# Kernel tuning notes

Hardware: AMD Instinct MI355X
Metric: run time of the kernel (lower is better)

The kernel has to match this reference:

```python
import jax, jax.numpy as jnp
import numpy as np

N_NODES = 100000
N_EDGES = 1600000
F_IN = 16
F_OUT = 16
N_BASIS = 4  # per spatial dim; basisTerms = [4, 4]


def linear_basis(u, n):
    """Piecewise-linear (hat) basis, n terms on [-1, 1]. u: [E] -> [E, n]."""
    centers = jnp.linspace(-1.0, 1.0, n, dtype=u.dtype)
    dx = 2.0 / (n - 1)
    return jnp.maximum(0.0, 1.0 - jnp.abs(u[:, None] - centers[None, :]) / dx)


def setup_inputs() -> dict:
    key = jax.random.key(0)
    k1, k2, k3, k4, k5 = jax.random.split(key, 5)
    x = jax.random.normal(k1, (N_NODES, F_IN), dtype=jnp.float32)
    edge_index = jax.random.randint(k2, (2, N_EDGES), 0, N_NODES, dtype=jnp.int64)
    # relative positions normalized to [-1, 1]^2 (as in initializeWeights2D)
    edge_attr = jax.random.uniform(k3, (N_EDGES, 2), dtype=jnp.float32,
                                   minval=-1.0, maxval=1.0)
    # weight: [*basisTerms, inputFeatures, outputFeatures], uniform(-0.05, 0.05)
    weight = jax.random.uniform(k4, (N_BASIS, N_BASIS, F_IN, F_OUT),
                                dtype=jnp.float32, minval=-0.05, maxval=0.05)
    return {"x": x, "edge_index": edge_index, "edge_attr": edge_attr,
            "weight": weight}


def reference(x, edge_index, edge_attr, weight):
    """BasisConvLayer forward, mode='conv', linear basis, no bias/activations.

    For each edge e=(i<-j): msg_e = sum_{u,v} b_u(dx) b_v(dy) * (x_j @ W[u,v]);
    out[i] = sum over incoming edges of msg_e.
    """
    row, col = edge_index[0], edge_index[1]
    x_j = x[col]                                   # [E, F_in] gather
    bx = linear_basis(edge_attr[:, 0], N_BASIS)    # [E, nB]
    by = linear_basis(edge_attr[:, 1], N_BASIS)    # [E, nB]
    # outer product of 1D bases -> [E, nB*nB] interpolation coefficients
    t = (bx[:, :, None] * by[:, None, :]).reshape(-1, N_BASIS * N_BASIS)
    w_flat = weight.reshape(N_BASIS * N_BASIS, F_IN, F_OUT)
    # accumulate over the small fixed basis-term set to avoid [E, Fin, Fout]
    msg = jnp.zeros((x_j.shape[0], F_OUT), dtype=x.dtype)
    for k in range(N_BASIS * N_BASIS):
        msg = msg + t[:, k, None] * (x_j @ w_flat[k])
    out = jax.ops.segment_sum(msg, row, num_segments=N_NODES)  # scatter-add
    return out
```

## Files before the change

### kernel.cpp

```cpp
#include <hip/hip_runtime.h>

#define N_NODES 100000
#define N_EDGES 1600000
#define F 16

#define EDGES_PER_BLOCK 512
#define GROUPS_PER_WAVE 8

#define OUT_FLOAT4 ((N_NODES * F) / 4)

typedef __attribute__((ext_vector_type(8))) short bf16x8;
typedef __attribute__((ext_vector_type(4))) float f32x4;

__global__ __launch_bounds__(256) void zero_out_kernel(float4* __restrict__ out) {
    int i = blockIdx.x * 256 + threadIdx.x;
    if (i < OUT_FLOAT4) out[i] = make_float4(0.f, 0.f, 0.f, 0.f);
}

__device__ __forceinline__ unsigned pk_bf16(float lo, float hi) {
    unsigned r;
    asm("v_cvt_pk_bf16_f32 %0, %1, %2" : "=v"(r) : "v"(lo), "v"(hi));
    return r;
}

__global__ __launch_bounds__(256) void basis_conv_mfma(
    const float* __restrict__ x,
    const int*   __restrict__ edge_index,
    const float* __restrict__ edge_attr,
    const float* __restrict__ weight,
    float*       __restrict__ out)
{
    const int lane = threadIdx.x & 63;
    const int wid  = threadIdx.x >> 6;
    const int e15  = lane & 15;
    const int fo   = lane & 15;
    const int c    = lane >> 4;
    const int hv   = c >> 1;
    const int i0   = (c & 1) * 8;

    bf16x8 bw[8];
#pragma unroll
    for (int m = 0; m < 8; ++m) {
        const float* wp = weight + (2 * m + hv) * 256 + i0 * 16 + fo;
        union { bf16x8 v; unsigned u[4]; } bb;
#pragma unroll
        for (int p = 0; p < 4; ++p)
            bb.u[p] = pk_bf16(wp[(2 * p) * 16], wp[(2 * p + 1) * 16]);
        bw[m] = bb.v;
    }

    const int wbase = blockIdx.x * EDGES_PER_BLOCK + wid * (16 * GROUPS_PER_WAVE);

#pragma unroll 1
    for (int g = 0; g < GROUPS_PER_WAVE; ++g) {
        const int eg = wbase + g * 16;

        const int col   = edge_index[N_EDGES + eg + e15];
        const float2 at = ((const float2*)edge_attr)[eg + e15];

        float fu = (at.x + 1.0f) * 1.5f;
        int iu = (int)fu; iu = iu < 0 ? 0 : (iu > 2 ? 2 : iu);
        const float wu1 = fu - (float)iu, wu0 = 1.0f - wu1;
        float fv = (at.y + 1.0f) * 1.5f;
        int iv = (int)fv; iv = iv < 0 ? 0 : (iv > 2 ? 2 : iv);
        const float wv1 = fv - (float)iv, wv0 = 1.0f - wv1;

        const float bu0 = iu == 0 ? wu0 : 0.f;
        const float bu1 = iu == 0 ? wu1 : (iu == 1 ? wu0 : 0.f);
        const float bu2 = iu == 2 ? wu0 : (iu == 1 ? wu1 : 0.f);
        const float bu3 = iu == 2 ? wu1 : 0.f;
        const float bv0 = iv == 0 ? wv0 : 0.f;
        const float bv1 = iv == 0 ? wv1 : (iv == 1 ? wv0 : 0.f);
        const float bv2 = iv == 2 ? wv0 : (iv == 1 ? wv1 : 0.f);
        const float bv3 = iv == 2 ? wv1 : 0.f;

        const float bvE = hv ? bv1 : bv0;
        const float bvO = hv ? bv3 : bv2;

        const float4* xv = (const float4*)(x + (size_t)col * 16 + i0);
        const float4 xa = xv[0], xb = xv[1];

        f32x4 acc0 = {0.f, 0.f, 0.f, 0.f};
        f32x4 acc1 = {0.f, 0.f, 0.f, 0.f};
#pragma unroll
        for (int m = 0; m < 8; ++m) {
            const float bu = (m >> 1) == 0 ? bu0 : (m >> 1) == 1 ? bu1
                           : (m >> 1) == 2 ? bu2 : bu3;
            const float t = bu * ((m & 1) ? bvO : bvE);
            union { bf16x8 v; unsigned u[4]; } aa;
            aa.u[0] = pk_bf16(t * xa.x, t * xa.y);
            aa.u[1] = pk_bf16(t * xa.z, t * xa.w);
            aa.u[2] = pk_bf16(t * xb.x, t * xb.y);
            aa.u[3] = pk_bf16(t * xb.z, t * xb.w);
            if (m & 1)
                acc1 = __builtin_amdgcn_mfma_f32_16x16x32_bf16(aa.v, bw[m], acc1, 0, 0, 0);
            else
                acc0 = __builtin_amdgcn_mfma_f32_16x16x32_bf16(aa.v, bw[m], acc0, 0, 0, 0);
        }
        const f32x4 acc = acc0 + acc1;

        const int4 r4 = *(const int4*)(edge_index + eg + 4 * c);
        unsafeAtomicAdd(out + (size_t)r4.x * 16 + fo, acc.x);
        unsafeAtomicAdd(out + (size_t)r4.y * 16 + fo, acc.y);
        unsafeAtomicAdd(out + (size_t)r4.z * 16 + fo, acc.z);
        unsafeAtomicAdd(out + (size_t)r4.w * 16 + fo, acc.w);
    }
}

extern "C" void kernel_launch(void* const* d_in, const int* in_sizes, int n_in,
                              void* d_out, int out_size, void* d_ws, size_t ws_size,
                              hipStream_t stream) {
    const float* x  = (const float*)d_in[0];
    const int*   ei = (const int*)d_in[1];
    const float* ea = (const float*)d_in[2];
    const float* w  = (const float*)d_in[3];
    float* out = (float*)d_out;
    (void)out_size; (void)d_ws; (void)ws_size; (void)in_sizes; (void)n_in;

    zero_out_kernel<<<(OUT_FLOAT4 + 255) / 256, 256, 0, stream>>>((float4*)out);

    const int blocks = N_EDGES / EDGES_PER_BLOCK;
    basis_conv_mfma<<<blocks, 256, 0, stream>>>(x, ei, ea, w, out);
}
```

Baseline: 165.6 us.

## Software-pipeline edge index, attribute and x-gather loads across groups

Adds a software pipeline to the per-wave group loop. Edge indices, attributes and destination rows are prefetched two groups ahead, and the gathered x row one group ahead, so global-memory latency overlaps the MFMA and atomic work of the current group. The prefetch index is clamped to stay in bounds, which makes the last iterations issue redundant loads. The extra live registers may lower occupancy.

```diff
diff --git a/kernel.cpp b/kernel.cpp
--- a/kernel.cpp
+++ b/kernel.cpp
@@ -51,17 +51,36 @@
 
     const int wbase = blockIdx.x * EDGES_PER_BLOCK + wid * (16 * GROUPS_PER_WAVE);
 
+    int col0, col1; float2 at0, at1; int4 r40, r41;
+    float4 xa0, xb0;
+    {
+        const int eg0 = wbase;
+        col0 = edge_index[N_EDGES + eg0 + e15];
+        at0  = ((const float2*)edge_attr)[eg0 + e15];
+        r40  = *(const int4*)(edge_index + eg0 + 4 * c);
+        const float4* xv = (const float4*)(x + (size_t)col0 * 16 + i0);
+        xa0 = xv[0]; xb0 = xv[1];
+        const int eg1 = wbase + 16;
+        col1 = edge_index[N_EDGES + eg1 + e15];
+        at1  = ((const float2*)edge_attr)[eg1 + e15];
+        r41  = *(const int4*)(edge_index + eg1 + 4 * c);
+    }
+
 #pragma unroll 1
     for (int g = 0; g < GROUPS_PER_WAVE; ++g) {
-        const int eg = wbase + g * 16;
+        const float4* xv1 = (const float4*)(x + (size_t)col1 * 16 + i0);
+        const float4 xa1 = xv1[0], xb1 = xv1[1];
 
-        const int col   = edge_index[N_EDGES + eg + e15];
-        const float2 at = ((const float2*)edge_attr)[eg + e15];
+        int eg2 = wbase + (g + 2) * 16;
+        eg2 = eg2 > (N_EDGES - 16) ? (N_EDGES - 16) : eg2;
+        const int   col2 = edge_index[N_EDGES + eg2 + e15];
+        const float2 at2 = ((const float2*)edge_attr)[eg2 + e15];
+        const int4  r42  = *(const int4*)(edge_index + eg2 + 4 * c);
 
-        float fu = (at.x + 1.0f) * 1.5f;
+        float fu = (at0.x + 1.0f) * 1.5f;
         int iu = (int)fu; iu = iu < 0 ? 0 : (iu > 2 ? 2 : iu);
         const float wu1 = fu - (float)iu, wu0 = 1.0f - wu1;
-        float fv = (at.y + 1.0f) * 1.5f;
+        float fv = (at0.y + 1.0f) * 1.5f;
         int iv = (int)fv; iv = iv < 0 ? 0 : (iv > 2 ? 2 : iv);
         const float wv1 = fv - (float)iv, wv0 = 1.0f - wv1;
 
@@ -77,9 +96,6 @@
         const float bvE = hv ? bv1 : bv0;
         const float bvO = hv ? bv3 : bv2;
 
-        const float4* xv = (const float4*)(x + (size_t)col * 16 + i0);
-        const float4 xa = xv[0], xb = xv[1];
-
         f32x4 acc0 = {0.f, 0.f, 0.f, 0.f};
         f32x4 acc1 = {0.f, 0.f, 0.f, 0.f};
 #pragma unroll
@@ -88,10 +104,10 @@
                            : (m >> 1) == 2 ? bu2 : bu3;
             const float t = bu * ((m & 1) ? bvO : bvE);
             union { bf16x8 v; unsigned u[4]; } aa;
-            aa.u[0] = pk_bf16(t * xa.x, t * xa.y);
-            aa.u[1] = pk_bf16(t * xa.z, t * xa.w);
-            aa.u[2] = pk_bf16(t * xb.x, t * xb.y);
-            aa.u[3] = pk_bf16(t * xb.z, t * xb.w);
+            aa.u[0] = pk_bf16(t * xa0.x, t * xa0.y);
+            aa.u[1] = pk_bf16(t * xa0.z, t * xa0.w);
+            aa.u[2] = pk_bf16(t * xb0.x, t * xb0.y);
+            aa.u[3] = pk_bf16(t * xb0.z, t * xb0.w);
             if (m & 1)
                 acc1 = __builtin_amdgcn_mfma_f32_16x16x32_bf16(aa.v, bw[m], acc1, 0, 0, 0);
             else
@@ -99,11 +115,14 @@
         }
         const f32x4 acc = acc0 + acc1;
 
-        const int4 r4 = *(const int4*)(edge_index + eg + 4 * c);
-        unsafeAtomicAdd(out + (size_t)r4.x * 16 + fo, acc.x);
-        unsafeAtomicAdd(out + (size_t)r4.y * 16 + fo, acc.y);
-        unsafeAtomicAdd(out + (size_t)r4.z * 16 + fo, acc.z);
-        unsafeAtomicAdd(out + (size_t)r4.w * 16 + fo, acc.w);
+        unsafeAtomicAdd(out + (size_t)r40.x * 16 + fo, acc.x);
+        unsafeAtomicAdd(out + (size_t)r40.y * 16 + fo, acc.y);
+        unsafeAtomicAdd(out + (size_t)r40.z * 16 + fo, acc.z);
+        unsafeAtomicAdd(out + (size_t)r40.w * 16 + fo, acc.w);
+
+        col0 = col1; at0 = at1; r40 = r41;
+        xa0 = xa1;  xb0 = xb1;
+        col1 = col2; at1 = at2; r41 = r42;
     }
 }
 
```

Measured after the change: 162.0 us, median of 2. 2.1% less time.

## Software-pipeline edge gathers two iterations ahead and process two groups per iteration

Applied to the files above, without the earlier changes.

Restructures the per-wave loop so each iteration handles two 16-edge groups, with the x-row gather prefetched one iteration ahead and the column/attribute loads two iterations ahead. The aim is to hide the latency of the dependent index-then-gather loads behind the MFMA work and atomics of the current groups. It also adds launch_bounds occupancy hint of 4 blocks. In exchange it raises register pressure, which the occupancy hint may force into spills, and it clamps prefetch addresses at the array end, so the tail does some redundant loads.

```diff
diff --git a/kernel.cpp b/kernel.cpp
--- a/kernel.cpp
+++ b/kernel.cpp
@@ -5,7 +5,7 @@
 #define F 16
 
 #define EDGES_PER_BLOCK 512
-#define GROUPS_PER_WAVE 8
+#define ITERS 4
 
 #define OUT_FLOAT4 ((N_NODES * F) / 4)
 
@@ -23,7 +23,7 @@
     return r;
 }
 
-__global__ __launch_bounds__(256) void basis_conv_mfma(
+__global__ __launch_bounds__(256, 4) void basis_conv_mfma(
     const float* __restrict__ x,
     const int*   __restrict__ edge_index,
     const float* __restrict__ edge_attr,
@@ -42,68 +42,112 @@
 #pragma unroll
     for (int m = 0; m < 8; ++m) {
         const float* wp = weight + (2 * m + hv) * 256 + i0 * 16 + fo;
-        union { bf16x8 v; unsigned u[4]; } bb;
+        union { bf16x8 v; unsigned w[4]; } bb;
 #pragma unroll
         for (int p = 0; p < 4; ++p)
-            bb.u[p] = pk_bf16(wp[(2 * p) * 16], wp[(2 * p + 1) * 16]);
+            bb.w[p] = pk_bf16(wp[(2 * p) * 16], wp[(2 * p + 1) * 16]);
         bw[m] = bb.v;
     }
 
-    const int wbase = blockIdx.x * EDGES_PER_BLOCK + wid * (16 * GROUPS_PER_WAVE);
+    const int wbase = blockIdx.x * EDGES_PER_BLOCK + wid * (32 * ITERS);
+
+    float2 at0[2], at1[2];
+    int    col1[2];
+    float4 xa0[2], xb0[2];
+
+    {
+#pragma unroll
+        for (int u = 0; u < 2; ++u) {
+            const int egA = wbase + u * 16;
+            const int col0 = edge_index[N_EDGES + egA + e15];
+            at0[u] = ((const float2*)edge_attr)[egA + e15];
+            const float4* xv = (const float4*)(x + (size_t)col0 * 16 + i0);
+            xa0[u] = xv[0]; xb0[u] = xv[1];
+            const int egB = wbase + 32 + u * 16;
+            col1[u] = edge_index[N_EDGES + egB + e15];
+            at1[u]  = ((const float2*)edge_attr)[egB + e15];
+        }
+    }
 
 #pragma unroll 1
-    for (int g = 0; g < GROUPS_PER_WAVE; ++g) {
-        const int eg = wbase + g * 16;
+    for (int g = 0; g < ITERS; ++g) {
+        int4 r40[2];
+#pragma unroll
+        for (int u = 0; u < 2; ++u)
+            r40[u] = *(const int4*)(edge_index + (wbase + g * 32 + u * 16) + 4 * c);
 
-        const int col   = edge_index[N_EDGES + eg + e15];
-        const float2 at = ((const float2*)edge_attr)[eg + e15];
+        float4 xa1[2], xb1[2];
+#pragma unroll
+        for (int u = 0; u < 2; ++u) {
+            const float4* xv = (const float4*)(x + (size_t)col1[u] * 16 + i0);
+            xa1[u] = xv[0]; xb1[u] = xv[1];
+        }
 
-        float fu = (at.x + 1.0f) * 1.5f;
-        int iu = (int)fu; iu = iu < 0 ? 0 : (iu > 2 ? 2 : iu);
-        const float wu1 = fu - (float)iu, wu0 = 1.0f - wu1;
-        float fv = (at.y + 1.0f) * 1.5f;
-        int iv = (int)fv; iv = iv < 0 ? 0 : (iv > 2 ? 2 : iv);
-        const float wv1 = fv - (float)iv, wv0 = 1.0f - wv1;
+        int col2[2]; float2 at2[2];
+#pragma unroll
+        for (int u = 0; u < 2; ++u) {
+            int eg2 = wbase + (g + 2) * 32 + u * 16;
+            eg2 = eg2 > (N_EDGES - 16) ? (N_EDGES - 16) : eg2;
+            col2[u] = edge_index[N_EDGES + eg2 + e15];
+            at2[u]  = ((const float2*)edge_attr)[eg2 + e15];
+        }
 
-        const float bu0 = iu == 0 ? wu0 : 0.f;
-        const float bu1 = iu == 0 ? wu1 : (iu == 1 ? wu0 : 0.f);
-        const float bu2 = iu == 2 ? wu0 : (iu == 1 ? wu1 : 0.f);
-        const float bu3 = iu == 2 ? wu1 : 0.f;
-        const float bv0 = iv == 0 ? wv0 : 0.f;
-        const float bv1 = iv == 0 ? wv1 : (iv == 1 ? wv0 : 0.f);
-        const float bv2 = iv == 2 ? wv0 : (iv == 1 ? wv1 : 0.f);
-        const float bv3 = iv == 2 ? wv1 : 0.f;
+        float bu_[2][4], bvE_[2], bvO_[2];
+#pragma unroll
+        for (int u = 0; u < 2; ++u) {
+            float fu = (at0[u].x + 1.0f) * 1.5f;
+            int iu = (int)fu; iu = iu < 0 ? 0 : (iu > 2 ? 2 : iu);
+            const float wu1 = fu - (float)iu, wu0 = 1.0f - wu1;
+            float fv = (at0[u].y + 1.0f) * 1.5f;
+            int iv = (int)fv; iv = iv < 0 ? 0 : (iv > 2 ? 2 : iv);
+            const float wv1 = fv - (float)iv, wv0 = 1.0f - wv1;
 
-        const float bvE = hv ? bv1 : bv0;
-        const float bvO = hv ? bv3 : bv2;
+            bu_[u][0] = iu == 0 ? wu0 : 0.f;
+            bu_[u][1] = iu == 0 ? wu1 : (iu == 1 ? wu0 : 0.f);
+            bu_[u][2] = iu == 2 ? wu0 : (iu == 1 ? wu1 : 0.f);
+            bu_[u][3] = iu == 2 ? wu1 : 0.f;
+            const float bv0 = iv == 0 ? wv0 : 0.f;
+            const float bv1 = iv == 0 ? wv1 : (iv == 1 ? wv0 : 0.f);
+            const float bv2 = iv == 2 ? wv0 : (iv == 1 ? wv1 : 0.f);
+            const float bv3 = iv == 2 ? wv1 : 0.f;
+            bvE_[u] = hv ? bv1 : bv0;
+            bvO_[u] = hv ? bv3 : bv2;
+        }
 
-        const float4* xv = (const float4*)(x + (size_t)col * 16 + i0);
-        const float4 xa = xv[0], xb = xv[1];
-
-        f32x4 acc0 = {0.f, 0.f, 0.f, 0.f};
-        f32x4 acc1 = {0.f, 0.f, 0.f, 0.f};
+        f32x4 accE[2] = {{0.f,0.f,0.f,0.f},{0.f,0.f,0.f,0.f}};
+        f32x4 accO[2] = {{0.f,0.f,0.f,0.f},{0.f,0.f,0.f,0.f}};
 #pragma unroll
         for (int m = 0; m < 8; ++m) {
-            const float bu = (m >> 1) == 0 ? bu0 : (m >> 1) == 1 ? bu1
-                           : (m >> 1) == 2 ? bu2 : bu3;
-            const float t = bu * ((m & 1) ? bvO : bvE);
-            union { bf16x8 v; unsigned u[4]; } aa;
-            aa.u[0] = pk_bf16(t * xa.x, t * xa.y);
-            aa.u[1] = pk_bf16(t * xa.z, t * xa.w);
-            aa.u[2] = pk_bf16(t * xb.x, t * xb.y);
-            aa.u[3] = pk_bf16(t * xb.z, t * xb.w);
-            if (m & 1)
-                acc1 = __builtin_amdgcn_mfma_f32_16x16x32_bf16(aa.v, bw[m], acc1, 0, 0, 0);
-            else
-                acc0 = __builtin_amdgcn_mfma_f32_16x16x32_bf16(aa.v, bw[m], acc0, 0, 0, 0);
+#pragma unroll
+            for (int u = 0; u < 2; ++u) {
+                const float t = bu_[u][m >> 1] * ((m & 1) ? bvO_[u] : bvE_[u]);
+                union { bf16x8 v; unsigned w[4]; } aa;
+                aa.w[0] = pk_bf16(t * xa0[u].x, t * xa0[u].y);
+                aa.w[1] = pk_bf16(t * xa0[u].z, t * xa0[u].w);
+                aa.w[2] = pk_bf16(t * xb0[u].x, t * xb0[u].y);
+                aa.w[3] = pk_bf16(t * xb0[u].z, t * xb0[u].w);
+                if (m & 1)
+                    accO[u] = __builtin_amdgcn_mfma_f32_16x16x32_bf16(aa.v, bw[m], accO[u], 0, 0, 0);
+                else
+                    accE[u] = __builtin_amdgcn_mfma_f32_16x16x32_bf16(aa.v, bw[m], accE[u], 0, 0, 0);
+            }
         }
-        const f32x4 acc = acc0 + acc1;
 
-        const int4 r4 = *(const int4*)(edge_index + eg + 4 * c);
-        unsafeAtomicAdd(out + (size_t)r4.x * 16 + fo, acc.x);
-        unsafeAtomicAdd(out + (size_t)r4.y * 16 + fo, acc.y);
-        unsafeAtomicAdd(out + (size_t)r4.z * 16 + fo, acc.z);
-        unsafeAtomicAdd(out + (size_t)r4.w * 16 + fo, acc.w);
+#pragma unroll
+        for (int u = 0; u < 2; ++u) {
+            const f32x4 acc = accE[u] + accO[u];
+            unsafeAtomicAdd(out + (size_t)r40[u].x * 16 + fo, acc.x);
+            unsafeAtomicAdd(out + (size_t)r40[u].y * 16 + fo, acc.y);
+            unsafeAtomicAdd(out + (size_t)r40[u].z * 16 + fo, acc.z);
+            unsafeAtomicAdd(out + (size_t)r40[u].w * 16 + fo, acc.w);
+        }
+
+#pragma unroll
+        for (int u = 0; u < 2; ++u) {
+            at0[u] = at1[u];
+            xa0[u] = xa1[u]; xb0[u] = xb1[u];
+            col1[u] = col2[u]; at1[u] = at2[u];
+        }
     }
 }
 
```

Result: no change. 164.7 us (-0.5%).
